# Optimization experiments

Hardware: AMD Instinct MI355X
Metric: run time of the kernel (lower is better)

## Reference

```python
import jax, jax.numpy as jnp
import numpy as np

N_NODES = 100000
N_EDGES = 250000
EMB = 300
LAYERS = 5
BN_EPS = 1e-5


def setup_inputs() -> dict:
    key = jax.random.key(0)
    ks = jax.random.split(key, 16)
    inp = {
        "x": jax.random.randint(ks[0], (N_NODES, 2), 0, 3, dtype=jnp.int64) if jax.config.jax_enable_x64 else jax.random.randint(ks[0], (N_NODES, 2), 0, 3, dtype=jnp.int32),
        "edge_index": jax.random.randint(ks[1], (2, N_EDGES), 0, N_NODES, dtype=jnp.int32),
        "edge_attr": jax.random.randint(ks[2], (N_EDGES, 2), 0, 3, dtype=jnp.int32),
        "atom_emb1": jax.random.normal(ks[3], (120, EMB), jnp.float32) * 0.1,
        "atom_emb2": jax.random.normal(ks[4], (3, EMB), jnp.float32) * 0.1,
        "edge_emb1": jax.random.normal(ks[5], (LAYERS, 6, EMB), jnp.float32) * 0.1,
        "edge_emb2": jax.random.normal(ks[6], (LAYERS, 3, EMB), jnp.float32) * 0.1,
        "W1": jax.random.normal(ks[7], (LAYERS, EMB, 2 * EMB), jnp.float32) * (1.0 / np.sqrt(EMB)),
        "b1": jnp.zeros((LAYERS, 2 * EMB), jnp.float32),
        "W2": jax.random.normal(ks[8], (LAYERS, 2 * EMB, EMB), jnp.float32) * (1.0 / np.sqrt(2 * EMB)),
        "b2": jnp.zeros((LAYERS, EMB), jnp.float32),
        "gamma": jnp.ones((LAYERS, EMB), jnp.float32),
        "beta": jnp.zeros((LAYERS, EMB), jnp.float32),
    }
    return inp


def reference(x, edge_index, edge_attr, atom_emb1, atom_emb2, edge_emb1, edge_emb2,
              W1, b1, W2, b2, gamma, beta):
    N = x.shape[0]
    L = W1.shape[0]
    # AtomEncoder: sum of per-feature embeddings
    h = atom_emb1[x[:, 0]] + atom_emb2[x[:, 1]]  # [N, D]
    # add self loops (attr = (4, 0)); PyG: messages flow src=row0 -> dst=row1
    sl = jnp.arange(N, dtype=edge_index.dtype)
    src = jnp.concatenate([edge_index[0], sl])
    dst = jnp.concatenate([edge_index[1], sl])
    ea0 = jnp.concatenate([edge_attr[:, 0], jnp.full((N,), 4, edge_attr.dtype)])
    ea1 = jnp.concatenate([edge_attr[:, 1], jnp.zeros((N,), edge_attr.dtype)])
    for l in range(L):
        e = edge_emb1[l][ea0] + edge_emb2[l][ea1]           # [E+N, D]
        msg = h[src] + e                                     # gather + add
        agg = jax.ops.segment_sum(msg, dst, num_segments=N)  # scatter-add
        hmid = jax.nn.relu(agg @ W1[l] + b1[l])
        hout = hmid @ W2[l] + b2[l]
        mean = hout.mean(axis=0)
        var = hout.var(axis=0)
        hbn = (hout - mean) * jax.lax.rsqrt(var + BN_EPS) * gamma[l] + beta[l]
        h = hbn if l == L - 1 else jax.nn.relu(hbn)          # dropout ratio 0
    return h
```

## Files before the change

kernel.cpp:

```cpp
#include <hip/hip_runtime.h>
#include <hip/hip_bf16.h>

#define N_NODESC 100000
#define N_EDGESC 250000
#define EMB 300
#define LD 304
#define LD4 76
#define LAYERS 5
#define BN_EPS 1e-5f

#define K1 320
#define N1 640
#define K2 640
#define N2 384

#define NB_SCAN 391

typedef __attribute__((ext_vector_type(8))) short short8;
typedef __attribute__((ext_vector_type(4))) float f32x4;

#define GLOAD16(g, l) __builtin_amdgcn_global_load_lds( \
    (const __attribute__((address_space(1))) void*)(g), \
    (__attribute__((address_space(3))) void*)(l), 16, 0, 0)

__device__ __forceinline__ float4 f4add(float4 a, float4 b){
    return make_float4(a.x+b.x, a.y+b.y, a.z+b.z, a.w+b.w);
}
__device__ __forceinline__ unsigned short f2bf(float f){
    __hip_bfloat16 h = __float2bfloat16(f);
    return *(unsigned short*)&h;
}

__global__ void k_zero_i(int* p, int n){
    int i = blockIdx.x*blockDim.x + threadIdx.x;
    if(i < n) p[i] = 0;
}
__global__ void k_zero_f(float* p, int n){
    int i = blockIdx.x*blockDim.x + threadIdx.x;
    if(i < n) p[i] = 0.f;
}

__global__ void k_atom(const int* __restrict__ x,
                       const float* __restrict__ e1,
                       const float* __restrict__ e2,
                       float* __restrict__ h){
    int idx = blockIdx.x*blockDim.x + threadIdx.x;
    if(idx >= N_NODESC*LD4) return;
    int i = idx / LD4, c = idx % LD4;
    float4 v = make_float4(0,0,0,0);
    if(c < 75){
        int i0 = x[2*i], i1 = x[2*i+1];
        const float4* r1 = (const float4*)(e1 + (size_t)i0*EMB);
        const float4* r2 = (const float4*)(e2 + (size_t)i1*EMB);
        v = f4add(r1[c], r2[c]);
    }
    ((float4*)h)[idx] = v;
}

__global__ void k_etab(const float* __restrict__ e1,
                       const float* __restrict__ e2,
                       float* __restrict__ etab){
    int idx = blockIdx.x*blockDim.x + threadIdx.x;
    if(idx >= LAYERS*18*LD4) return;
    int l = idx / (18*LD4);
    int r = idx % (18*LD4);
    int c = r / LD4, f = r % LD4;
    float4 v = make_float4(0,0,0,0);
    if(f < 75){
        const float4* r1 = (const float4*)(e1 + (size_t)(l*6 + c/3)*EMB);
        const float4* r2 = (const float4*)(e2 + (size_t)(l*3 + c%3)*EMB);
        v = f4add(r1[f], r2[f]);
    }
    ((float4*)etab)[idx] = v;
}

__global__ void k_prepw1(const float* __restrict__ W1, unsigned short* __restrict__ wb){
    int idx = blockIdx.x*blockDim.x + threadIdx.x;
    if(idx >= LAYERS*N1*K1) return;
    int l = idx / (N1*K1);
    int r = idx % (N1*K1);
    int n = r / K1, k = r % K1;
    float v = (n < 600 && k < EMB) ? W1[((size_t)l*EMB + k)*600 + n] : 0.f;
    wb[idx] = f2bf(v);
}
__global__ void k_prepw2(const float* __restrict__ W2, unsigned short* __restrict__ wb){
    int idx = blockIdx.x*blockDim.x + threadIdx.x;
    if(idx >= LAYERS*N2*K2) return;
    int l = idx / (N2*K2);
    int r = idx % (N2*K2);
    int n = r / K2, k = r % K2;
    float v = (n < EMB && k < 600) ? W2[((size_t)l*600 + k)*EMB + n] : 0.f;
    wb[idx] = f2bf(v);
}
__global__ void k_prepb1(const float* __restrict__ b1, float* __restrict__ bp){
    int idx = blockIdx.x*blockDim.x + threadIdx.x;
    if(idx >= LAYERS*N1) return;
    int l = idx / N1, n = idx % N1;
    bp[idx] = (n < 600) ? b1[(size_t)l*600 + n] : 0.f;
}

__global__ void k_deg(const int* __restrict__ ei, int* __restrict__ deg){
    int e = blockIdx.x*blockDim.x + threadIdx.x;
    if(e >= N_EDGESC) return;
    atomicAdd(&deg[ei[N_EDGESC + e]], 1);
}

__global__ void k_bsum(const int* __restrict__ deg, int* __restrict__ bsum){
    int g = blockIdx.x*256 + threadIdx.x;
    int v = (g < N_NODESC) ? deg[g] : 0;
    #pragma unroll
    for(int o=32;o>0;o>>=1) v += __shfl_down(v, o);
    __shared__ int sw[4];
    if((threadIdx.x & 63) == 0) sw[threadIdx.x>>6] = v;
    __syncthreads();
    if(threadIdx.x == 0) bsum[blockIdx.x] = sw[0]+sw[1]+sw[2]+sw[3];
}

__global__ void k_bscan(const int* __restrict__ bsum, int* __restrict__ bpre,
                        int* __restrict__ offs){
    __shared__ int sh[512];
    int t = threadIdx.x;
    int v = (t < NB_SCAN) ? bsum[t] : 0;
    sh[t] = v; __syncthreads();
    for(int o=1;o<512;o<<=1){
        int u = (t >= o) ? sh[t-o] : 0;
        __syncthreads();
        sh[t] += u;
        __syncthreads();
    }
    if(t < NB_SCAN) bpre[t] = sh[t] - v;
    if(t == NB_SCAN-1) offs[N_NODESC] = sh[t];
}

__global__ void k_offs(const int* __restrict__ deg, const int* __restrict__ bpre,
                       int* __restrict__ offs, int* __restrict__ cursor){
    __shared__ int sh[256];
    int t = threadIdx.x;
    int g = blockIdx.x*256 + t;
    int v = (g < N_NODESC) ? deg[g] : 0;
    sh[t] = v; __syncthreads();
    for(int o=1;o<256;o<<=1){
        int u = (t >= o) ? sh[t-o] : 0;
        __syncthreads();
        sh[t] += u;
        __syncthreads();
    }
    if(g < N_NODESC){
        int e = bpre[blockIdx.x] + sh[t] - v;
        offs[g] = e; cursor[g] = e;
    }
}

__global__ void k_fill(const int* __restrict__ ei, const int* __restrict__ ea,
                       int* __restrict__ cursor,
                       int* __restrict__ csr_src, int* __restrict__ csr_ea){
    int e = blockIdx.x*blockDim.x + threadIdx.x;
    if(e >= N_EDGESC) return;
    int d = ei[N_EDGESC + e];
    int p = atomicAdd(&cursor[d], 1);
    csr_src[p] = ei[e];
    csr_ea[p]  = ea[2*e]*3 + ea[2*e+1];
}

template<int BN>
__global__ void k_aggT(const float* __restrict__ src, const float* __restrict__ etab_l,
                       const float* __restrict__ aff,
                       const int* __restrict__ offs, const int* __restrict__ csr_src,
                       const int* __restrict__ csr_ea, unsigned short* __restrict__ agg){
    int idx = blockIdx.x*blockDim.x + threadIdx.x;
    if(idx >= N_NODESC*80) return;
    int i = idx / 80, c = idx % 80;
    ushort4 out;
    if(c < 75){
        const float4* s4 = (const float4*)src;
        const float4* et = (const float4*)etab_l;
        const int stride = BN ? 75 : LD4;
        float4 a4, b4;
        if(BN){ a4 = ((const float4*)aff)[c]; b4 = ((const float4*)aff)[75 + c]; }
        #define LOADV(s_, v_) { float4 x_ = s4[(size_t)(s_)*stride + c];          \
            if(BN){ v_.x = fmaxf(fmaf(x_.x,a4.x,b4.x),0.f);                       \
                    v_.y = fmaxf(fmaf(x_.y,a4.y,b4.y),0.f);                       \
                    v_.z = fmaxf(fmaf(x_.z,a4.z,b4.z),0.f);                       \
                    v_.w = fmaxf(fmaf(x_.w,a4.w,b4.w),0.f); } else v_ = x_; }
        float4 v;
        LOADV(i, v)
        float4 acc = f4add(v, et[12*LD4 + c]);
        int j0 = offs[i], j1 = offs[i+1];
        for(int j=j0; j<j1; j++){
            int s = csr_src[j];
            int t = csr_ea[j];
            LOADV(s, v)
            acc = f4add(acc, f4add(v, et[t*LD4 + c]));
        }
        #undef LOADV
        out.x = f2bf(acc.x); out.y = f2bf(acc.y);
        out.z = f2bf(acc.z); out.w = f2bf(acc.w);
    } else {
        out.x = out.y = out.z = out.w = 0;
    }
    *(ushort4*)(agg + (size_t)i*K1 + c*4) = out;
}

__global__ void k_bnaff(const float* __restrict__ stats, const float* __restrict__ g,
                        const float* __restrict__ bt, float* __restrict__ aff){
    int c = blockIdx.x*blockDim.x + threadIdx.x;
    if(c >= EMB) return;
    const float inv_n = 1.0f/(float)N_NODESC;
    float m = stats[c]*inv_n;
    float var = stats[EMB + c]*inv_n - m*m;
    float a = g[c]*rsqrtf(var + BN_EPS);
    aff[c] = a;
    aff[EMB + c] = bt[c] - m*a;
}

template<int EPI, int KS, int NX>
__global__ __launch_bounds__(512) void k_mgemm(
    const unsigned short* __restrict__ A,
    const unsigned short* __restrict__ Bt,
    const float* __restrict__ bias,
    void* __restrict__ Cptr, int M, int ldc,
    float* __restrict__ stats, int nwg)
{
    __shared__ char smem_c[3*24576 + 4096];
    unsigned short* smem_u = (unsigned short*)smem_c;

    int bid = blockIdx.x;
    int q = nwg >> 3, r = nwg & 7;
    int xcd = bid & 7, lo = bid >> 3;
    int wg = (xcd < r) ? (xcd*(q+1) + lo) : (r*(q+1) + (xcd - r)*q + lo);
    int bx = wg % NX, by = wg / NX;
    int m0 = by*256, n0 = bx*128;

    const int tid = threadIdx.x;
    const int wv = tid >> 6, ln = tid & 63;
    const int wvm = wv >> 1, wvn = wv & 1;
    const int lr = ln & 15, hi = ln >> 4;

    const int rS = tid >> 2, cS = tid & 3;
    int gA0 = m0 + rS;       if(gA0 >= M) gA0 = M-1;
    int gA1 = m0 + 128 + rS; if(gA1 >= M) gA1 = M-1;
    const unsigned short* srcA0 = A  + (size_t)gA0*(KS*32) + ((cS ^ ((rS>>1)&3))<<3);
    const unsigned short* srcA1 = A  + (size_t)gA1*(KS*32) + ((cS ^ ((rS>>1)&3))<<3);
    const unsigned short* srcB  = Bt + (size_t)(n0 + rS)*(KS*32) + ((cS ^ ((rS>>1)&3))<<3);

    f32x4 acc[4][4] = {};

    #define STAGE(t) { \
        char* db_ = smem_c + ((t)%3)*24576; \
        GLOAD16(srcA0 + (t)*32, db_ + tid*16); \
        GLOAD16(srcA1 + (t)*32, db_ + (512 + tid)*16); \
        GLOAD16(srcB  + (t)*32, db_ + 16384 + tid*16); }

    STAGE(0)
    __builtin_amdgcn_sched_barrier(0);
    STAGE(1)
    __builtin_amdgcn_sched_barrier(0);

    int offA[4], offB[4];
    #pragma unroll
    for(int m=0;m<4;m++){
        int row = wvm*64 + m*16 + lr;
        offA[m] = row*32 + ((hi ^ ((row>>1)&3))<<3);
    }
    #pragma unroll
    for(int n=0;n<4;n++){
        int brow = wvn*64 + n*16 + lr;
        offB[n] = 8192 + brow*32 + ((hi ^ ((brow>>1)&3))<<3);
    }

    #pragma unroll
    for(int kc=0; kc<KS; kc++){
        if(kc == KS-1) asm volatile("s_waitcnt vmcnt(0) lgkmcnt(0)" ::: "memory");
        else           asm volatile("s_waitcnt vmcnt(3) lgkmcnt(0)" ::: "memory");
        __builtin_amdgcn_s_barrier();
        __builtin_amdgcn_sched_barrier(0);
        if(kc+2 < KS) STAGE(kc+2)
        const unsigned short* bufu = smem_u + (kc%3)*12288;
        short8 av[4], bv[4];
        #pragma unroll
        for(int m=0;m<4;m++) av[m] = *(const short8*)(bufu + offA[m]);
        #pragma unroll
        for(int n=0;n<4;n++) bv[n] = *(const short8*)(bufu + offB[n]);
        __builtin_amdgcn_s_setprio(1);
        #pragma unroll
        for(int m=0;m<4;m++)
            #pragma unroll
            for(int n=0;n<4;n++)
                acc[m][n] = __builtin_amdgcn_mfma_f32_16x16x32_bf16(
                                av[m], bv[n], acc[m][n], 0, 0, 0);
        __builtin_amdgcn_s_setprio(0);
    }
    #undef STAGE

    __syncthreads();

    if(EPI == 0){
        unsigned short* Cs = smem_u;
        unsigned short* Cb = (unsigned short*)Cptr;
        #pragma unroll
        for(int n=0;n<4;n++){
            int col = wvn*64 + n*16 + lr;
            float bsv = bias[n0 + col];
            #pragma unroll
            for(int m=0;m<4;m++){
                #pragma unroll
                for(int j=0;j<4;j++){
                    int row = wvm*64 + m*16 + hi*4 + j;
                    Cs[row*136 + col] = f2bf(fmaxf(acc[m][n][j] + bsv, 0.f));
                }
            }
        }
        __syncthreads();
        #pragma unroll
        for(int i=0;i<8;i++){
            int id = i*512 + tid;
            int rr = id >> 4, ch = id & 15;
            int gr = m0 + rr;
            if(gr < M)
                *(short8*)(Cb + (size_t)gr*ldc + n0 + ch*8) =
                    *(const short8*)(Cs + rr*136 + ch*8);
        }
    } else {
        float* Cf = (float*)Cptr;
        float* red = (float*)(smem_c + 3*24576);
        #pragma unroll
        for(int n=0;n<4;n++){
            int col = n0 + wvn*64 + n*16 + lr;
            bool cok = (col < EMB);
            float bsv = cok ? bias[col] : 0.f;
            float sS = 0.f, sQ = 0.f;
            #pragma unroll
            for(int m=0;m<4;m++){
                #pragma unroll
                for(int j=0;j<4;j++){
                    int row = m0 + wvm*64 + m*16 + hi*4 + j;
                    if(cok && row < M){
                        float v = acc[m][n][j] + bsv;
                        sS += v; sQ += v*v;
                    }
                }
            }
            sS += __shfl_xor(sS, 16); sQ += __shfl_xor(sQ, 16);
            sS += __shfl_xor(sS, 32); sQ += __shfl_xor(sQ, 32);
            if(hi == 0){
                red[(wv*4+n)*16 + lr]       = sS;
                red[512 + (wv*4+n)*16 + lr] = sQ;
            }
        }
        __syncthreads();
        if(tid < 128){
            int twvn = tid >> 6, tn = (tid >> 4) & 3, tlr = tid & 15;
            float S = 0.f, Q = 0.f;
            #pragma unroll
            for(int wm2=0; wm2<4; wm2++){
                int w = wm2*2 + twvn;
                S += red[(w*4+tn)*16 + tlr];
                Q += red[512 + (w*4+tn)*16 + tlr];
            }
            int c2 = n0 + twvn*64 + tn*16 + tlr;
            if(c2 < EMB){
                atomicAdd(&stats[c2], S);
                atomicAdd(&stats[EMB + c2], Q);
            }
        }
        __syncthreads();
        float* Cs = (float*)smem_c;
        #pragma unroll
        for(int qq=0; qq<4; qq++){
            if(wvm == qq){
                #pragma unroll
                for(int n=0;n<4;n++){
                    int col = wvn*64 + n*16 + lr;
                    float bsv = (n0 + col < EMB) ? bias[n0 + col] : 0.f;
                    #pragma unroll
                    for(int m=0;m<4;m++){
                        #pragma unroll
                        for(int j=0;j<4;j++){
                            int rl = m*16 + hi*4 + j;
                            Cs[rl*132 + col] = acc[m][n][j] + bsv;
                        }
                    }
                }
            }
            __syncthreads();
            #pragma unroll
            for(int i=0;i<4;i++){
                int id = i*512 + tid;
                int rr = id >> 5, c4 = id & 31;
                int col = n0 + c4*4;
                int gr = m0 + qq*64 + rr;
                if(col < EMB && gr < M)
                    *(float4*)(Cf + (size_t)gr*ldc + col) =
                        *(const float4*)(Cs + rr*132 + c4*4);
            }
            __syncthreads();
        }
    }
}

__global__ void k_bnapply(const float* __restrict__ X, const float* __restrict__ stats,
                          const float* __restrict__ g, const float* __restrict__ bt,
                          float* __restrict__ dout){
    int idx = blockIdx.x*blockDim.x + threadIdx.x;
    if(idx >= N_NODESC*75) return;
    int i = idx / 75, c = idx % 75;
    const float4* X4 = (const float4*)X;
    float4 v  = X4[(size_t)i*75 + c];
    float4 s  = ((const float4*)stats)[c];
    float4 q  = ((const float4*)stats)[75 + c];
    float4 gg = ((const float4*)g)[c];
    float4 bb = ((const float4*)bt)[c];
    const float inv_n = 1.0f/(float)N_NODESC;
    #define BN1(f) { float m = s.f*inv_n; float var = q.f*inv_n - m*m;          \
                     float r = rsqrtf(var + BN_EPS);                             \
                     v.f = (v.f - m)*r*gg.f + bb.f; }
    BN1(x) BN1(y) BN1(z) BN1(w)
    #undef BN1
    ((float4*)dout)[(size_t)i*75 + c] = v;
}

extern "C" void kernel_launch(void* const* d_in, const int* in_sizes, int n_in,
                              void* d_out, int out_size, void* d_ws, size_t ws_size,
                              hipStream_t stream) {
    const int*   x     = (const int*)d_in[0];
    const int*   ei    = (const int*)d_in[1];
    const int*   ea    = (const int*)d_in[2];
    const float* aemb1 = (const float*)d_in[3];
    const float* aemb2 = (const float*)d_in[4];
    const float* eemb1 = (const float*)d_in[5];
    const float* eemb2 = (const float*)d_in[6];
    const float* W1    = (const float*)d_in[7];
    const float* b1    = (const float*)d_in[8];
    const float* W2    = (const float*)d_in[9];
    const float* b2    = (const float*)d_in[10];
    const float* gamma = (const float*)d_in[11];
    const float* beta  = (const float*)d_in[12];
    float* dout = (float*)d_out;

    float* h      = (float*)d_ws;
    float* bias1p = h + (size_t)N_NODESC*LD;
    float* etab   = bias1p + LAYERS*N1;
    float* stats  = etab + LAYERS*18*LD;
    float* aff    = stats + 640;
    unsigned short* agg  = (unsigned short*)(aff + 640);
    unsigned short* hmid = agg  + (size_t)N_NODESC*K1;
    unsigned short* wb1t = hmid + (size_t)N_NODESC*N1;
    unsigned short* wb2t = wb1t + (size_t)LAYERS*N1*K1;
    int*   deg     = (int*)(wb2t + (size_t)LAYERS*N2*K2);
    int*   offs    = deg    + N_NODESC;
    int*   cursor  = offs   + N_NODESC + 1;
    int*   csr_src = cursor + N_NODESC + 1;
    int*   csr_ea  = csr_src + N_EDGESC;
    int*   bsum    = csr_ea + N_EDGESC;
    int*   bpre    = bsum + NB_SCAN;

    const int nb_nf4 = (N_NODESC*LD4 + 255)/256;

    k_atom<<<nb_nf4, 256, 0, stream>>>(x, aemb1, aemb2, h);
    k_etab<<<(LAYERS*18*LD4 + 255)/256, 256, 0, stream>>>(eemb1, eemb2, etab);
    k_prepw1<<<(LAYERS*N1*K1 + 255)/256, 256, 0, stream>>>(W1, wb1t);
    k_prepw2<<<(LAYERS*N2*K2 + 255)/256, 256, 0, stream>>>(W2, wb2t);
    k_prepb1<<<(LAYERS*N1 + 255)/256, 256, 0, stream>>>(b1, bias1p);
    k_zero_i<<<(N_NODESC + 255)/256, 256, 0, stream>>>(deg, N_NODESC);
    k_deg<<<(N_EDGESC + 255)/256, 256, 0, stream>>>(ei, deg);
    k_bsum<<<NB_SCAN, 256, 0, stream>>>(deg, bsum);
    k_bscan<<<1, 512, 0, stream>>>(bsum, bpre, offs);
    k_offs<<<NB_SCAN, 256, 0, stream>>>(deg, bpre, offs, cursor);
    k_fill<<<(N_EDGESC + 255)/256, 256, 0, stream>>>(ei, ea, cursor, csr_src, csr_ea);

    const int MT2 = (N_NODESC + 255)/256;
    const int nwg1 = 5*MT2, nwg2 = 3*MT2;
    const int nb_agg = (N_NODESC*80 + 255)/256;
    for(int l=0; l<LAYERS; l++){
        if(l == 0)
            k_aggT<0><<<nb_agg, 256, 0, stream>>>(
                h, etab, stats , offs, csr_src, csr_ea, agg);
        else
            k_aggT<1><<<nb_agg, 256, 0, stream>>>(
                dout, etab + (size_t)l*18*LD, aff, offs, csr_src, csr_ea, agg);
        k_zero_f<<<(2*EMB + 255)/256, 256, 0, stream>>>(stats, 2*EMB);
        k_mgemm<0, 10, 5><<<nwg1, 512, 0, stream>>>(
            agg, wb1t + (size_t)l*N1*K1, bias1p + (size_t)l*N1,
            hmid, N_NODESC, N1, nullptr, nwg1);
        k_mgemm<1, 20, 3><<<nwg2, 512, 0, stream>>>(
            hmid, wb2t + (size_t)l*N2*K2, b2 + (size_t)l*EMB,
            dout, N_NODESC, EMB, stats, nwg2);
        if(l < LAYERS-1)
            k_bnaff<<<2, 256, 0, stream>>>(stats, gamma + (size_t)l*EMB,
                                           beta + (size_t)l*EMB, aff);
        else
            k_bnapply<<<(N_NODESC*75 + 255)/256, 256, 0, stream>>>(
                dout, stats, gamma + (size_t)l*EMB, beta + (size_t)l*EMB, dout);
    }
}
```

Baseline: 1.438 ms.

## Shrink GEMM M-tile to 128 and split K across two wave groups

The MFMA GEMM tile drops from 256x128 to 128x128. The eight waves now form two K-split groups that take alternating K-chunks, and their partial accumulators are combined through LDS before the epilogue. Shared memory per block shrinks and launch bounds ask for more resident blocks, which doubles the number of workgroups. This is meant to improve occupancy and load balance across CUs. The cost is lower per-tile reuse of B, an extra LDS reduction with its barriers, and idle waves during each K step.

```diff
diff --git a/kernel.cpp b/kernel.cpp
--- a/kernel.cpp
+++ b/kernel.cpp
@@ -214,14 +214,14 @@
 }
 
 template<int EPI, int KS, int NX>
-__global__ __launch_bounds__(512) void k_mgemm(
+__global__ __launch_bounds__(512, 4) void k_mgemm(
     const unsigned short* __restrict__ A,
     const unsigned short* __restrict__ Bt,
     const float* __restrict__ bias,
     void* __restrict__ Cptr, int M, int ldc,
     float* __restrict__ stats, int nwg)
 {
-    __shared__ char smem_c[3*24576 + 4096];
+    __shared__ char smem_c[3*16384 + 4096];
     unsigned short* smem_u = (unsigned short*)smem_c;
 
     int bid = blockIdx.x;
@@ -229,27 +229,26 @@
     int xcd = bid & 7, lo = bid >> 3;
     int wg = (xcd < r) ? (xcd*(q+1) + lo) : (r*(q+1) + (xcd - r)*q + lo);
     int bx = wg % NX, by = wg / NX;
-    int m0 = by*256, n0 = bx*128;
+    int m0 = by*128, n0 = bx*128;
 
     const int tid = threadIdx.x;
     const int wv = tid >> 6, ln = tid & 63;
-    const int wvm = wv >> 1, wvn = wv & 1;
+    const int ks = wv >> 2;
+    const int p  = wv & 3;
+    const int wvm = p >> 1, wvn = p & 1;
     const int lr = ln & 15, hi = ln >> 4;
 
     const int rS = tid >> 2, cS = tid & 3;
-    int gA0 = m0 + rS;       if(gA0 >= M) gA0 = M-1;
-    int gA1 = m0 + 128 + rS; if(gA1 >= M) gA1 = M-1;
-    const unsigned short* srcA0 = A  + (size_t)gA0*(KS*32) + ((cS ^ ((rS>>1)&3))<<3);
-    const unsigned short* srcA1 = A  + (size_t)gA1*(KS*32) + ((cS ^ ((rS>>1)&3))<<3);
-    const unsigned short* srcB  = Bt + (size_t)(n0 + rS)*(KS*32) + ((cS ^ ((rS>>1)&3))<<3);
+    int gA = m0 + rS; if(gA >= M) gA = M-1;
+    const unsigned short* srcA = A  + (size_t)gA*(KS*32)        + ((cS ^ ((rS>>1)&3))<<3);
+    const unsigned short* srcB = Bt + (size_t)(n0 + rS)*(KS*32) + ((cS ^ ((rS>>1)&3))<<3);
 
     f32x4 acc[4][4] = {};
 
     #define STAGE(t) { \
-        char* db_ = smem_c + ((t)%3)*24576; \
-        GLOAD16(srcA0 + (t)*32, db_ + tid*16); \
-        GLOAD16(srcA1 + (t)*32, db_ + (512 + tid)*16); \
-        GLOAD16(srcB  + (t)*32, db_ + 16384 + tid*16); }
+        char* db_ = smem_c + ((t)%3)*16384; \
+        GLOAD16(srcA + (t)*32, db_ + tid*16); \
+        GLOAD16(srcB + (t)*32, db_ + 8192 + tid*16); }
 
     STAGE(0)
     __builtin_amdgcn_sched_barrier(0);
@@ -265,54 +264,87 @@
     #pragma unroll
     for(int n=0;n<4;n++){
         int brow = wvn*64 + n*16 + lr;
-        offB[n] = 8192 + brow*32 + ((hi ^ ((brow>>1)&3))<<3);
+        offB[n] = 4096 + brow*32 + ((hi ^ ((brow>>1)&3))<<3);
     }
 
     #pragma unroll
     for(int kc=0; kc<KS; kc++){
         if(kc == KS-1) asm volatile("s_waitcnt vmcnt(0) lgkmcnt(0)" ::: "memory");
-        else           asm volatile("s_waitcnt vmcnt(3) lgkmcnt(0)" ::: "memory");
+        else           asm volatile("s_waitcnt vmcnt(2) lgkmcnt(0)" ::: "memory");
         __builtin_amdgcn_s_barrier();
         __builtin_amdgcn_sched_barrier(0);
         if(kc+2 < KS) STAGE(kc+2)
-        const unsigned short* bufu = smem_u + (kc%3)*12288;
-        short8 av[4], bv[4];
+        if((kc & 1) == ks){
+            const unsigned short* bufu = smem_u + (kc%3)*8192;
+            short8 av[4], bv[4];
+            #pragma unroll
+            for(int m=0;m<4;m++) av[m] = *(const short8*)(bufu + offA[m]);
+            #pragma unroll
+            for(int n=0;n<4;n++) bv[n] = *(const short8*)(bufu + offB[n]);
+            __builtin_amdgcn_s_setprio(1);
+            #pragma unroll
+            for(int m=0;m<4;m++)
+                #pragma unroll
+                for(int n=0;n<4;n++)
+                    acc[m][n] = __builtin_amdgcn_mfma_f32_16x16x32_bf16(
+                                    av[m], bv[n], acc[m][n], 0, 0, 0);
+            __builtin_amdgcn_s_setprio(0);
+        }
+    }
+    #undef STAGE
+
+    __syncthreads();
+
+    {
+        float* cmb = (float*)smem_c;
         #pragma unroll
-        for(int m=0;m<4;m++) av[m] = *(const short8*)(bufu + offA[m]);
-        #pragma unroll
-        for(int n=0;n<4;n++) bv[n] = *(const short8*)(bufu + offB[n]);
-        __builtin_amdgcn_s_setprio(1);
-        #pragma unroll
-        for(int m=0;m<4;m++)
-            #pragma unroll
-            for(int n=0;n<4;n++)
-                acc[m][n] = __builtin_amdgcn_mfma_f32_16x16x32_bf16(
-                                av[m], bv[n], acc[m][n], 0, 0, 0);
-        __builtin_amdgcn_s_setprio(0);
-    }
-    #undef STAGE
-
-    __syncthreads();
+        for(int r2=0; r2<2; r2++){
+            if(ks == 1 && wvm == r2){
+                int base = wvn*4352;
+                #pragma unroll
+                for(int m=0;m<4;m++)
+                    #pragma unroll
+                    for(int n=0;n<4;n++)
+                        #pragma unroll
+                        for(int j=0;j<4;j++)
+                            cmb[base + (m*16 + hi*4 + j)*68 + n*16 + lr] = acc[m][n][j];
+            }
+            __syncthreads();
+            if(ks == 0 && wvm == r2){
+                int base = wvn*4352;
+                #pragma unroll
+                for(int m=0;m<4;m++)
+                    #pragma unroll
+                    for(int n=0;n<4;n++)
+                        #pragma unroll
+                        for(int j=0;j<4;j++)
+                            acc[m][n][j] += cmb[base + (m*16 + hi*4 + j)*68 + n*16 + lr];
+            }
+            __syncthreads();
+        }
+    }
 
     if(EPI == 0){
         unsigned short* Cs = smem_u;
         unsigned short* Cb = (unsigned short*)Cptr;
+        if(ks == 0){
+            #pragma unroll
+            for(int n=0;n<4;n++){
+                int col = wvn*64 + n*16 + lr;
+                float bsv = bias[n0 + col];
+                #pragma unroll
+                for(int m=0;m<4;m++){
+                    #pragma unroll
+                    for(int j=0;j<4;j++){
+                        int row = wvm*64 + m*16 + hi*4 + j;
+                        Cs[row*136 + col] = f2bf(fmaxf(acc[m][n][j] + bsv, 0.f));
+                    }
+                }
+            }
+        }
+        __syncthreads();
         #pragma unroll
-        for(int n=0;n<4;n++){
-            int col = wvn*64 + n*16 + lr;
-            float bsv = bias[n0 + col];
-            #pragma unroll
-            for(int m=0;m<4;m++){
-                #pragma unroll
-                for(int j=0;j<4;j++){
-                    int row = wvm*64 + m*16 + hi*4 + j;
-                    Cs[row*136 + col] = f2bf(fmaxf(acc[m][n][j] + bsv, 0.f));
-                }
-            }
-        }
-        __syncthreads();
-        #pragma unroll
-        for(int i=0;i<8;i++){
+        for(int i=0;i<4;i++){
             int id = i*512 + tid;
             int rr = id >> 4, ch = id & 15;
             int gr = m0 + rr;
@@ -322,29 +354,31 @@
         }
     } else {
         float* Cf = (float*)Cptr;
-        float* red = (float*)(smem_c + 3*24576);
-        #pragma unroll
-        for(int n=0;n<4;n++){
-            int col = n0 + wvn*64 + n*16 + lr;
-            bool cok = (col < EMB);
-            float bsv = cok ? bias[col] : 0.f;
-            float sS = 0.f, sQ = 0.f;
-            #pragma unroll
-            for(int m=0;m<4;m++){
+        float* red = (float*)(smem_c + 3*16384);
+        if(ks == 0){
+            #pragma unroll
+            for(int n=0;n<4;n++){
+                int col = n0 + wvn*64 + n*16 + lr;
+                bool cok = (col < EMB);
+                float bsv = cok ? bias[col] : 0.f;
+                float sS = 0.f, sQ = 0.f;
                 #pragma unroll
-                for(int j=0;j<4;j++){
-                    int row = m0 + wvm*64 + m*16 + hi*4 + j;
-                    if(cok && row < M){
-                        float v = acc[m][n][j] + bsv;
-                        sS += v; sQ += v*v;
+                for(int m=0;m<4;m++){
+                    #pragma unroll
+                    for(int j=0;j<4;j++){
+                        int row = m0 + wvm*64 + m*16 + hi*4 + j;
+                        if(cok && row < M){
+                            float v = acc[m][n][j] + bsv;
+                            sS += v; sQ += v*v;
+                        }
                     }
                 }
-            }
-            sS += __shfl_xor(sS, 16); sQ += __shfl_xor(sQ, 16);
-            sS += __shfl_xor(sS, 32); sQ += __shfl_xor(sQ, 32);
-            if(hi == 0){
-                red[(wv*4+n)*16 + lr]       = sS;
-                red[512 + (wv*4+n)*16 + lr] = sQ;
+                sS += __shfl_xor(sS, 16); sQ += __shfl_xor(sQ, 16);
+                sS += __shfl_xor(sS, 32); sQ += __shfl_xor(sQ, 32);
+                if(hi == 0){
+                    red[(wv*4+n)*16 + lr]       = sS;
+                    red[512 + (wv*4+n)*16 + lr] = sQ;
+                }
             }
         }
         __syncthreads();
@@ -352,7 +386,7 @@
             int twvn = tid >> 6, tn = (tid >> 4) & 3, tlr = tid & 15;
             float S = 0.f, Q = 0.f;
             #pragma unroll
-            for(int wm2=0; wm2<4; wm2++){
+            for(int wm2=0; wm2<2; wm2++){
                 int w = wm2*2 + twvn;
                 S += red[(w*4+tn)*16 + tlr];
                 Q += red[512 + (w*4+tn)*16 + tlr];
@@ -366,8 +400,8 @@
         __syncthreads();
         float* Cs = (float*)smem_c;
         #pragma unroll
-        for(int qq=0; qq<4; qq++){
-            if(wvm == qq){
+        for(int half=0; half<2; half++){
+            if(ks == 0 && wvm == half){
                 #pragma unroll
                 for(int n=0;n<4;n++){
                     int col = wvn*64 + n*16 + lr;
@@ -388,7 +422,7 @@
                 int id = i*512 + tid;
                 int rr = id >> 5, c4 = id & 31;
                 int col = n0 + c4*4;
-                int gr = m0 + qq*64 + rr;
+                int gr = m0 + half*64 + rr;
                 if(col < EMB && gr < M)
                     *(float4*)(Cf + (size_t)gr*ldc + col) =
                         *(const float4*)(Cs + rr*132 + c4*4);
@@ -468,8 +502,8 @@
     k_offs<<<NB_SCAN, 256, 0, stream>>>(deg, bpre, offs, cursor);
     k_fill<<<(N_EDGESC + 255)/256, 256, 0, stream>>>(ei, ea, cursor, csr_src, csr_ea);
 
-    const int MT2 = (N_NODESC + 255)/256;
-    const int nwg1 = 5*MT2, nwg2 = 3*MT2;
+    const int MT = (N_NODESC + 127)/128;
+    const int nwg1 = 5*MT, nwg2 = 3*MT;
     const int nb_agg = (N_NODESC*80 + 255)/256;
     for(int l=0; l<LAYERS; l++){
         if(l == 0)
```

After: 1.477 ms. +2.7%, slower.
